# Optimization experiments

Hardware: AMD Instinct MI355X
Metric: run time of the kernel (lower is better)

Reference implementation:

```python
import jax, jax.numpy as jnp
import numpy as np

GROUPS = 8
EPS = 1e-5
PERM_IN = {'x': (0, 2, 4, 1, 3), 'y': (0, 2, 3, 1, 4), 'seq': (0, 3, 4, 1, 2)}
PERM_OUT = {'x': (0, 3, 1, 4, 2), 'y': (0, 3, 1, 2, 4), 'seq': (0, 3, 4, 1, 2)}


def bn_train(x, gamma, beta, axis=1):
    """Training-mode batch norm: normalize over all axes except `axis`."""
    axes = tuple(i for i in range(x.ndim) if i != axis)
    mean = x.mean(axes, keepdims=True)
    var = x.var(axes, keepdims=True)
    shp = [1] * x.ndim
    shp[axis] = x.shape[axis]
    return (x - mean) * jax.lax.rsqrt(var + EPS) * gamma.reshape(shp) + beta.reshape(shp)


def axial_attn(x, qkv_w, gq, bq, gs, bs, go, bo, direction):
    # x: (N, C, seq, H, W)
    x = jnp.transpose(x, PERM_IN[direction])
    N, seq, W, C, H = x.shape
    B = N * seq * W
    xf = x.reshape(B, C, H)
    # 1x1 conv1d qkv projection + BN over channels
    qkv = jnp.einsum('oc,bch->boh', qkv_w, xf)            # (B, 2C, H)
    qkv = bn_train(qkv, gq, bq, axis=1)
    gp = C // GROUPS                                       # group_planes
    qkv = qkv.reshape(B, GROUPS, 2 * gp, H)
    q = qkv[:, :, : gp // 2]
    k = qkv[:, :, gp // 2: gp]
    v = qkv[:, :, gp:]
    qk = jnp.einsum('bgci,bgcj->bgij', q, k)               # (B, g, H, H)
    qk = bn_train(qk, gs, bs, axis=1)
    sim = jax.nn.softmax(qk, axis=3)
    sv = jnp.einsum('bgij,bgcj->bgci', sim, v)             # (B, g, gp, H)
    sv = bn_train(sv.reshape(B, C, H), go, bo, axis=1)
    out = sv.reshape(N, seq, W, C, H)
    return jnp.transpose(out, PERM_OUT[direction])


def setup_inputs() -> dict:
    key = jax.random.key(0)
    ks = jax.random.split(key, 4)
    N, C_in, seq, H, W = 2, 128, 16, 56, 56
    width = 64
    x = jax.random.normal(ks[0], (N, C_in, seq, H, W), jnp.float32)
    cd_w = jax.random.normal(ks[1], (width, C_in), jnp.float32) * (1.0 / np.sqrt(C_in))
    qkv_w = jax.random.normal(ks[2], (3, 2 * width, width), jnp.float32) * (1.0 / np.sqrt(width))
    cu_w = jax.random.normal(ks[3], (2 * width, width), jnp.float32) * (1.0 / np.sqrt(width))
    return {
        'x': x,
        'cd_w': cd_w,
        'bn1_g': jnp.ones((width,), jnp.float32),
        'bn1_b': jnp.zeros((width,), jnp.float32),
        'qkv_w': qkv_w,
        'bnq_g': jnp.ones((3, 2 * width), jnp.float32),
        'bnq_b': jnp.zeros((3, 2 * width), jnp.float32),
        'bns_g': jnp.ones((3, GROUPS), jnp.float32),
        'bns_b': jnp.zeros((3, GROUPS), jnp.float32),
        'bno_g': jnp.ones((3, width), jnp.float32),
        'bno_b': jnp.zeros((3, width), jnp.float32),
        'cu_w': cu_w,
        'bn2_g': jnp.ones((2 * width,), jnp.float32),
        'bn2_b': jnp.zeros((2 * width,), jnp.float32),
    }


def reference(x, cd_w, bn1_g, bn1_b, qkv_w, bnq_g, bnq_b, bns_g, bns_b,
              bno_g, bno_b, cu_w, bn2_g, bn2_b):
    identity = x
    out = jnp.einsum('oc,ncshw->noshw', cd_w, x)           # conv_down (1x1)
    out = jax.nn.relu(bn_train(out, bn1_g, bn1_b, axis=1))
    for i, d in enumerate(('x', 'y', 'seq')):              # height, width, seq axial passes
        out = axial_attn(out, qkv_w[i], bnq_g[i], bnq_b[i], bns_g[i], bns_b[i],
                         bno_g[i], bno_b[i], d)
    out = jax.nn.relu(out)
    out = jnp.einsum('oc,ncshw->noshw', cu_w, out)         # conv_up (1x1)
    out = bn_train(out, bn2_g, bn2_b, axis=1)
    return jax.nn.relu(out + identity)
```

## Files before the change

kernel.cpp:

```cpp
#include <hip/hip_runtime.h>

constexpr int SP = 16*56*56;
constexpr int P  = 2*SP;
constexpr float EPSV = 1e-5f;
constexpr float INVP = 1.f/100352.f;

constexpr size_t SZ_A   = (size_t)2*64*SP;
constexpr size_t OFF_A  = 0;
constexpr size_t OFF_C  = SZ_A;
constexpr size_t OFF_ST = OFF_C + SZ_A;
constexpr size_t OFF_P1 = 0;
constexpr size_t OFF_P2 = 65536;

__global__ void __launch_bounds__(256) kern_down(
    const float* __restrict__ x, const float* __restrict__ w,
    float* __restrict__ A, float* __restrict__ st)
{
  __shared__ float xs[128*64];
  __shared__ float wt[64*129];
  __shared__ float ssum[64], ssq[64];
  const int t = threadIdx.x;
  if (t < 64) { ssum[t] = 0.f; ssq[t] = 0.f; }
  const int p0 = blockIdx.x * 64;
  const int n = p0 / SP, rem = p0 % SP;
  const float* xb = x + (size_t)n*128*SP + rem;
  for (int e4 = t; e4 < 128*16; e4 += 256) {
    int c = e4 >> 4, p4 = (e4 & 15)*4;
    float4 v = *reinterpret_cast<const float4*>(xb + (size_t)c*SP + p4);
    *reinterpret_cast<float4*>(&xs[c*64 + p4]) = v;
  }
  for (int e4 = t; e4 < 64*32; e4 += 256) {
    int o = e4 >> 5, c4 = (e4 & 31)*4;
    float4 v = *reinterpret_cast<const float4*>(w + o*128 + c4);
    *reinterpret_cast<float4*>(&wt[o*129 + c4]) = v;
  }
  __syncthreads();
  const int og = t & 15, pg = t >> 4;
  float acc[4][4] = {};
  for (int c = 0; c < 128; ++c) {
    float xv[4], wv[4];
    #pragma unroll
    for (int j = 0; j < 4; ++j) xv[j] = xs[c*64 + pg*4 + j];
    #pragma unroll
    for (int i = 0; i < 4; ++i) wv[i] = wt[(og + 16*i)*129 + c];
    #pragma unroll
    for (int i = 0; i < 4; ++i) {
      #pragma unroll
      for (int j = 0; j < 4; ++j) acc[i][j] = fmaf(wv[i], xv[j], acc[i][j]);
    }
  }
  float* Ab = A + (size_t)n*64*SP + rem;
  #pragma unroll
  for (int i = 0; i < 4; ++i) {
    const int o = og + 16*i;
    float s1 = 0.f, s2 = 0.f;
    #pragma unroll
    for (int j = 0; j < 4; ++j) { float v = acc[i][j]; s1 += v; s2 += v*v; }
    float4 v4 = make_float4(acc[i][0], acc[i][1], acc[i][2], acc[i][3]);
    *reinterpret_cast<float4*>(Ab + (size_t)o*SP + pg*4) = v4;
    atomicAdd(&ssum[o], s1);
    atomicAdd(&ssq[o], s2);
  }
  __syncthreads();
  if (t < 64) { atomicAdd(&st[t], ssum[t]); atomicAdd(&st[64+t], ssq[t]); }
}

__global__ void __launch_bounds__(256) kern_tr(
    const float* __restrict__ A, float* __restrict__ At)
{
  __shared__ float tile[56*57];
  const size_t base = (size_t)blockIdx.x*3136;
  for (int e4 = threadIdx.x; e4 < 784; e4 += 256) {
    int e = e4*4, h = e/56, w = e%56;
    float4 v = *reinterpret_cast<const float4*>(A + base + e);
    tile[w*57+h] = v.x; tile[(w+1)*57+h] = v.y;
    tile[(w+2)*57+h] = v.z; tile[(w+3)*57+h] = v.w;
  }
  __syncthreads();
  for (int e4 = threadIdx.x; e4 < 784; e4 += 256) {
    int e = e4*4, w = e/56, h = e%56;
    float4 v = make_float4(tile[w*57+h], tile[w*57+h+1], tile[w*57+h+2], tile[w*57+h+3]);
    *reinterpret_cast<float4*>(At + base + e) = v;
  }
}

__global__ void __launch_bounds__(256) kern_tr2(
    const float* __restrict__ A, float* __restrict__ At2)
{
  __shared__ float tile[16*785];
  const int bid = blockIdx.x;
  const int slice = bid >> 2, hw0 = (bid & 3)*784;
  const float* Asrc = A + (size_t)slice*SP + hw0;
  for (int e4 = threadIdx.x; e4 < 3136; e4 += 256) {
    int s = e4/196, h4 = (e4%196)*4;
    float4 v = *reinterpret_cast<const float4*>(Asrc + (size_t)s*3136 + h4);
    tile[s*785 + h4]   = v.x; tile[s*785 + h4+1] = v.y;
    tile[s*785 + h4+2] = v.z; tile[s*785 + h4+3] = v.w;
  }
  __syncthreads();
  float* dst = At2 + ((size_t)slice*3136 + hw0)*16;
  for (int hw = threadIdx.x; hw < 784; hw += 256) {
    #pragma unroll
    for (int sq = 0; sq < 4; ++sq) {
      float4 v = make_float4(tile[(4*sq)*785 + hw], tile[(4*sq+1)*785 + hw],
                             tile[(4*sq+2)*785 + hw], tile[(4*sq+3)*785 + hw]);
      *reinterpret_cast<float4*>(dst + (size_t)hw*16 + sq*4) = v;
    }
  }
}

__global__ void __launch_bounds__(256) kern_up(
    const float* __restrict__ A, const float* __restrict__ w,
    float* __restrict__ U, float* __restrict__ st)
{
  __shared__ float xs[64*64];
  __shared__ float wt[128*65];
  __shared__ float ssum[128], ssq[128];
  const int t = threadIdx.x;
  if (t < 128) { ssum[t]=0.f; ssq[t]=0.f; }
  const int p0 = blockIdx.x*64;
  const int n = p0/SP, rem = p0%SP;
  const float* Ab = A + (size_t)n*64*SP + rem;
  for (int e4 = t; e4 < 64*16; e4 += 256) {
    int c = e4 >> 4, p4 = (e4 & 15)*4;
    float4 v = *reinterpret_cast<const float4*>(Ab + (size_t)c*SP + p4);
    v.x = fmaxf(v.x, 0.f); v.y = fmaxf(v.y, 0.f); v.z = fmaxf(v.z, 0.f); v.w = fmaxf(v.w, 0.f);
    *reinterpret_cast<float4*>(&xs[c*64 + p4]) = v;
  }
  for (int e4 = t; e4 < 128*16; e4 += 256) {
    int o = e4 >> 4, c4 = (e4 & 15)*4;
    float4 v = *reinterpret_cast<const float4*>(w + o*64 + c4);
    *reinterpret_cast<float4*>(&wt[o*65 + c4]) = v;
  }
  __syncthreads();
  const int og = t & 31, pg = t >> 5;
  float acc[4][8] = {};
  for (int c = 0; c < 64; ++c) {
    float xv[8];
    #pragma unroll
    for (int j = 0; j < 8; ++j) xv[j] = xs[c*64 + pg*8 + j];
    #pragma unroll
    for (int i = 0; i < 4; ++i) {
      float wv = wt[(og + 32*i)*65 + c];
      #pragma unroll
      for (int j = 0; j < 8; ++j) acc[i][j] = fmaf(wv, xv[j], acc[i][j]);
    }
  }
  float* Ub = U + (size_t)n*128*SP + rem;
  #pragma unroll
  for (int i = 0; i < 4; ++i) {
    const int o = og + 32*i;
    float s1=0.f, s2=0.f;
    #pragma unroll
    for (int j = 0; j < 8; ++j) { float v = acc[i][j]; s1 += v; s2 += v*v; }
    float4 a = make_float4(acc[i][0],acc[i][1],acc[i][2],acc[i][3]);
    float4 b = make_float4(acc[i][4],acc[i][5],acc[i][6],acc[i][7]);
    *reinterpret_cast<float4*>(Ub + (size_t)o*SP + pg*8)     = a;
    *reinterpret_cast<float4*>(Ub + (size_t)o*SP + pg*8 + 4) = b;
    atomicAdd(&ssum[o], s1); atomicAdd(&ssq[o], s2);
  }
  __syncthreads();
  if (t < 128) { atomicAdd(&st[t], ssum[t]); atomicAdd(&st[128+t], ssq[t]); }
}

template<bool FIRST>
__global__ void __launch_bounds__(256) kern_qkv(
    const float* __restrict__ src, const float* __restrict__ w,
    const float* __restrict__ st1, const float* __restrict__ g1,
    const float* __restrict__ b1,
    float* __restrict__ Bq, float* __restrict__ st)
{
  constexpr int H = 56;
  __shared__ float xs[64*H];
  __shared__ float wt[128*65];
  __shared__ float ssum[128], ssq[128];
  __shared__ float sc1s[64], sh1s[64];
  const int t = threadIdx.x;
  if (t < 128) { ssum[t]=0.f; ssq[t]=0.f; }
  if (FIRST) {
    if (t < 64) {
      float mean = st1[t]*INVP;
      float var  = st1[64+t]*INVP - mean*mean;
      float sc   = g1[t]*rsqrtf(var + EPSV);
      sc1s[t] = sc; sh1s[t] = b1[t] - mean*sc;
    }
    __syncthreads();
  }
  const int b = blockIdx.x;
  const int n = b/896, r = b%896, s = r/56, q = r%56;
  const size_t base = (size_t)n*64*SP + s*3136 + q*56;
  for (int e4 = t; e4 < 64*14; e4 += 256) {
    int c = e4/14, j4 = (e4%14)*4;
    float4 v = *reinterpret_cast<const float4*>(src + base + (size_t)c*SP + j4);
    if (FIRST) {
      float sc = sc1s[c], sh = sh1s[c];
      v.x = fmaxf(fmaf(v.x, sc, sh), 0.f); v.y = fmaxf(fmaf(v.y, sc, sh), 0.f);
      v.z = fmaxf(fmaf(v.z, sc, sh), 0.f); v.w = fmaxf(fmaf(v.w, sc, sh), 0.f);
    }
    xs[c*H + j4]   = v.x; xs[c*H + j4+1] = v.y;
    xs[c*H + j4+2] = v.z; xs[c*H + j4+3] = v.w;
  }
  for (int e4 = t; e4 < 128*16; e4 += 256) {
    int o = e4 >> 4, c4 = (e4 & 15)*4;
    float4 v = *reinterpret_cast<const float4*>(w + o*64 + c4);
    *reinterpret_cast<float4*>(&wt[o*65 + c4]) = v;
  }
  __syncthreads();
  const int og = t & 31, hg = t >> 5;
  float acc[4][7] = {};
  for (int c = 0; c < 64; ++c) {
    float xv[7];
    #pragma unroll
    for (int j = 0; j < 7; ++j) xv[j] = xs[c*H + hg*7 + j];
    #pragma unroll
    for (int i = 0; i < 4; ++i) {
      float wv = wt[(og + 32*i)*65 + c];
      #pragma unroll
      for (int j = 0; j < 7; ++j) acc[i][j] = fmaf(wv, xv[j], acc[i][j]);
    }
  }
  float* ob = Bq + (size_t)b*128*H;
  #pragma unroll
  for (int i = 0; i < 4; ++i) {
    const int o = og + 32*i;
    float s1=0.f, s2=0.f;
    #pragma unroll
    for (int j = 0; j < 7; ++j) {
      float v = acc[i][j];
      ob[o*H + hg*7 + j] = v;
      s1 += v; s2 += v*v;
    }
    atomicAdd(&ssum[o], s1); atomicAdd(&ssq[o], s2);
  }
  __syncthreads();
  if (t < 128) { atomicAdd(&st[t], ssum[t]); atomicAdd(&st[128+t], ssq[t]); }
}

__global__ void __launch_bounds__(256) kern_qkv2(
    const float* __restrict__ At2, const float* __restrict__ w,
    float* __restrict__ Bq, float* __restrict__ st)
{
  __shared__ float xs[64*64];
  __shared__ float wt[128*65];
  __shared__ float ssum[128], ssq[128];
  const int t = threadIdx.x;
  if (t < 128) { ssum[t]=0.f; ssq[t]=0.f; }
  const int b = blockIdx.x;
  const int n = b/784, r = b%784, y = r/14, w4 = (r%14)*4;
  for (int e4 = t; e4 < 1024; e4 += 256) {
    int c = e4 >> 4, rr = e4 & 15, wl = rr >> 2, s4 = (rr & 3)*4;
    float4 v = *reinterpret_cast<const float4*>(
        At2 + (((size_t)(n*64+c)*3136) + y*56 + w4 + wl)*16 + s4);
    *reinterpret_cast<float4*>(&xs[c*64 + wl*16 + s4]) = v;
  }
  for (int e4 = t; e4 < 128*16; e4 += 256) {
    int o = e4 >> 4, c4 = (e4 & 15)*4;
    float4 v = *reinterpret_cast<const float4*>(w + o*64 + c4);
    *reinterpret_cast<float4*>(&wt[o*65 + c4]) = v;
  }
  __syncthreads();
  const int og = t & 31, cg = t >> 5;
  float acc[4][8] = {};
  for (int c = 0; c < 64; ++c) {
    float xv[8];
    #pragma unroll
    for (int j = 0; j < 8; ++j) xv[j] = xs[c*64 + cg*8 + j];
    #pragma unroll
    for (int i = 0; i < 4; ++i) {
      float wv = wt[(og + 32*i)*65 + c];
      #pragma unroll
      for (int j = 0; j < 8; ++j) acc[i][j] = fmaf(wv, xv[j], acc[i][j]);
    }
  }
  const size_t b0 = (size_t)n*3136 + (size_t)y*56 + w4;
  #pragma unroll
  for (int i = 0; i < 4; ++i) {
    const int o = og + 32*i;
    float s1=0.f, s2=0.f;
    #pragma unroll
    for (int j = 0; j < 8; ++j) {
      int col = cg*8 + j, wl = col >> 4, s = col & 15;
      float v = acc[i][j];
      Bq[(b0 + wl)*2048 + o*16 + s] = v;
      s1 += v; s2 += v*v;
    }
    atomicAdd(&ssum[o], s1); atomicAdd(&ssq[o], s2);
  }
  __syncthreads();
  if (t < 128) { atomicAdd(&st[t], ssum[t]); atomicAdd(&st[128+t], ssq[t]); }
}

__global__ void __launch_bounds__(256) kern_redfin(
    const float* __restrict__ part, const float* __restrict__ g,
    const float* __restrict__ b, float* __restrict__ scsh,
    int nb, int nch, float invc)
{
  const int ch = blockIdx.x;
  const int t = threadIdx.x;
  float s1 = 0.f, s2 = 0.f;
  for (int i = t; i < nb; i += 256) {
    s1 += part[(size_t)i*2*nch + ch];
    s2 += part[(size_t)i*2*nch + nch + ch];
  }
  #pragma unroll
  for (int off = 32; off >= 1; off >>= 1) { s1 += __shfl_xor(s1, off); s2 += __shfl_xor(s2, off); }
  __shared__ float r1[4], r2[4];
  if ((t & 63) == 0) { r1[t>>6] = s1; r2[t>>6] = s2; }
  __syncthreads();
  if (t == 0) {
    float S1 = r1[0]+r1[1]+r1[2]+r1[3], S2 = r2[0]+r2[1]+r2[2]+r2[3];
    float mean = S1*invc, var = S2*invc - mean*mean;
    float sc = g[ch]*rsqrtf(var + EPSV);
    scsh[ch] = sc;
    scsh[nch + ch] = b[ch] - mean*sc;
  }
}

template<int H>
__global__ void __launch_bounds__(256) kern_pass1(
    const float* __restrict__ Bq, const float* __restrict__ stq,
    const float* __restrict__ gq, const float* __restrict__ bq,
    float* __restrict__ part)
{
  constexpr int PW = (H==16) ? 4 : 1;
  const int t = threadIdx.x;
  const int wave = t >> 6, lane = t & 63;
  const int sub = (PW==1) ? 0 : (lane >> 4);
  const int i = (PW==1) ? lane : (lane & 15);
  __shared__ float kls[4][4*H*PW];
  __shared__ float bs[16];
  __shared__ float qscs[128], qshs[128];
  if (t < 16) bs[t] = 0.f;
  if (t < 128) {
    float mean = stq[t]*INVP;
    float var  = stq[128+t]*INVP - mean*mean;
    float sc   = gq[t]*rsqrtf(var + EPSV);
    qscs[t] = sc; qshs[t] = bq[t] - mean*sc;
  }
  __syncthreads();
  float* klw = kls[wave];
  const int pair0 = (blockIdx.x*4 + wave)*PW;
  for (int e = lane; e < 4*H*PW; e += 64) {
    int sp = e / (4*H), r = e % (4*H);
    int c = r / H, j = r % H;
    int pr = pair0 + sp, bb = pr >> 3, g = pr & 7;
    int o = g*16 + 4 + c;
    klw[e] = fmaf(Bq[((size_t)bb*128 + o)*H + j], qscs[o], qshs[o]);
  }
  __syncthreads();
  const int pr = pair0 + sub, bb = pr >> 3, g = pr & 7;
  const float* kp = klw + sub*4*H;
  const bool act = (i < H);
  float q[4];
  #pragma unroll
  for (int c = 0; c < 4; ++c) {
    int o = g*16 + c;
    q[c] = act ? fmaf(Bq[((size_t)bb*128 + o)*H + i], qscs[o], qshs[o]) : 0.f;
  }
  float s1 = 0.f, s2 = 0.f;
  #pragma unroll
  for (int j = 0; j < H; ++j) {
    float s = q[0]*kp[j] + q[1]*kp[H+j] + q[2]*kp[2*H+j] + q[3]*kp[3*H+j];
    s1 += s; s2 += s*s;
  }
  #pragma unroll
  for (int off = (PW==1?32:8); off >= 1; off >>= 1) {
    s1 += __shfl_xor(s1, off);
    s2 += __shfl_xor(s2, off);
  }
  if ((lane & (PW==1?63:15)) == 0) { atomicAdd(&bs[g], s1); atomicAdd(&bs[8+g], s2); }
  __syncthreads();
  if (t < 16) part[(size_t)blockIdx.x*16 + t] = bs[t];
}

template<int H>
__global__ void __launch_bounds__(256) kern_attn(
    const float* __restrict__ Bq, const float* __restrict__ stq,
    const float* __restrict__ gq, const float* __restrict__ bq,
    const float* __restrict__ ssc,
    float* __restrict__ C, float* __restrict__ part)
{
  constexpr int PW = (H==16) ? 4 : 1;
  const int t = threadIdx.x;
  const int wave = t >> 6, lane = t & 63;
  const int sub = (PW==1) ? 0 : (lane >> 4);
  const int i = (PW==1) ? lane : (lane & 15);
  __shared__ float kv[4][12*H*PW];
  __shared__ float bsum[64], bsq[64];
  __shared__ float qscs[128], qshs[128];
  if (t < 64) { bsum[t] = 0.f; bsq[t] = 0.f; }
  if (t < 128) {
    float mean = stq[t]*INVP;
    float var  = stq[128+t]*INVP - mean*mean;
    float sc   = gq[t]*rsqrtf(var + EPSV);
    qscs[t] = sc; qshs[t] = bq[t] - mean*sc;
  }
  __syncthreads();
  float* kvw = kv[wave];
  const int pair0 = (blockIdx.x*4 + wave)*PW;
  for (int e = lane; e < 12*H*PW; e += 64) {
    int sp = e / (12*H), r = e % (12*H);
    int c = r / H, j = r % H;
    int pr = pair0 + sp, bb = pr >> 3, g = pr & 7;
    int o = g*16 + 4 + c;
    kvw[e] = fmaf(Bq[((size_t)bb*128 + o)*H + j], qscs[o], qshs[o]);
  }
  __syncthreads();
  const int pr = pair0 + sub, bb = pr >> 3, g = pr & 7;
  const float* kp = kvw + sub*12*H;
  const bool act = (i < H);
  float q[4];
  #pragma unroll
  for (int c = 0; c < 4; ++c) {
    int o = g*16 + c;
    q[c] = act ? fmaf(Bq[((size_t)bb*128 + o)*H + i], qscs[o], qshs[o]) : 0.f;
  }
  const float As = ssc[g];
  float m = -3.4e38f;
  for (int j = 0; j < H; ++j) {
    float s = As * (q[0]*kp[j] + q[1]*kp[H+j] + q[2]*kp[2*H+j] + q[3]*kp[3*H+j]);
    m = fmaxf(m, s);
  }
  float den = 0.f;
  float acc[8] = {};
  for (int j = 0; j < H; ++j) {
    float s = As * (q[0]*kp[j] + q[1]*kp[H+j] + q[2]*kp[2*H+j] + q[3]*kp[3*H+j]);
    float e = __expf(s - m);
    den += e;
    #pragma unroll
    for (int c = 0; c < 8; ++c) acc[c] = fmaf(e, kp[(4+c)*H + j], acc[c]);
  }
  const float inv = 1.f/den;
  #pragma unroll
  for (int c = 0; c < 8; ++c) {
    float vv = act ? acc[c]*inv : 0.f;
    if (act) C[((size_t)bb*64 + g*8 + c)*H + i] = vv;
    float s1 = vv, s2 = vv*vv;
    #pragma unroll
    for (int off = (PW==1?32:8); off >= 1; off >>= 1) {
      s1 += __shfl_xor(s1, off);
      s2 += __shfl_xor(s2, off);
    }
    if ((lane & (PW==1?63:15)) == 0) { atomicAdd(&bsum[g*8+c], s1); atomicAdd(&bsq[g*8+c], s2); }
  }
  __syncthreads();
  if (t < 64) {
    part[(size_t)blockIdx.x*128 + t]      = bsum[t];
    part[(size_t)blockIdx.x*128 + 64 + t] = bsq[t];
  }
}

__global__ void __launch_bounds__(256) kern_scat0(
    const float* __restrict__ C, const float* __restrict__ osc,
    const float* __restrict__ osh, float* __restrict__ A)
{
  __shared__ float tile[56*57];
  const int bid = blockIdx.x;
  const int c = bid & 63, s = (bid >> 6) & 15, n = bid >> 10;
  const float sc = osc[c], sh = osh[c];
  const size_t cb = ((size_t)(n*16+s)*56)*3584 + c*56;
  for (int e = threadIdx.x; e < 3136; e += 256) {
    int w = e/56, h = e%56;
    tile[w*57+h] = C[cb + (size_t)w*3584 + h];
  }
  __syncthreads();
  const size_t ab = ((size_t)(n*64+c)*16+s)*3136;
  for (int e = threadIdx.x; e < 3136; e += 256) {
    int h = e/56, w = e%56;
    A[ab + e] = fmaf(tile[w*57+h], sc, sh);
  }
}

__global__ void __launch_bounds__(256) kern_scat1(
    const float* __restrict__ C, const float* __restrict__ osc,
    const float* __restrict__ osh, float* __restrict__ A)
{
  const int e4 = blockIdx.x*256 + threadIdx.x;
  if (e4 >= 1792*64*14) return;
  const int w4 = (e4 % 14)*4, c = (e4/14) & 63, b = e4 / (14*64);
  const int n = b/896, r = b%896, s = r/56, y = r%56;
  const float sc = osc[c], sh = osh[c];
  float4 v = *reinterpret_cast<const float4*>(C + ((size_t)b*64 + c)*56 + w4);
  v.x = fmaf(v.x, sc, sh); v.y = fmaf(v.y, sc, sh);
  v.z = fmaf(v.z, sc, sh); v.w = fmaf(v.w, sc, sh);
  *reinterpret_cast<float4*>(A + ((size_t)(n*64+c)*16+s)*3136 + y*56 + w4) = v;
}

__global__ void __launch_bounds__(256) kern_scat2(
    const float* __restrict__ C, const float* __restrict__ osc,
    const float* __restrict__ osh, float* __restrict__ A)
{
  __shared__ float tile[56*17];
  const int bid = blockIdx.x;
  const int y = bid % 56, c = (bid/56) & 63, n = bid / 3584;
  const float sc = osc[c], sh = osh[c];
  const size_t cb = ((size_t)(n*56+y)*56)*1024 + c*16;
  for (int e = threadIdx.x; e < 896; e += 256) {
    int w = e >> 4, s = e & 15;
    tile[w*17+s] = C[cb + (size_t)w*1024 + s];
  }
  __syncthreads();
  const size_t ab = (size_t)(n*64+c)*16*3136 + y*56;
  for (int e = threadIdx.x; e < 896; e += 256) {
    int s = e/56, w = e%56;
    A[ab + (size_t)s*3136 + w] = fmaf(tile[w*17+s], sc, sh);
  }
}

__global__ void __launch_bounds__(256) kern_final(
    float* __restrict__ U, const float* __restrict__ x,
    const float* __restrict__ st2, const float* __restrict__ g2,
    const float* __restrict__ b2, float* __restrict__ out)
{
  __shared__ float scs[128], shs[128];
  const int t = threadIdx.x;
  if (t < 128) {
    float mean = st2[t]*INVP;
    float var  = st2[128+t]*INVP - mean*mean;
    float sc   = g2[t]*rsqrtf(var + EPSV);
    scs[t] = sc; shs[t] = b2[t] - mean*sc;
  }
  __syncthreads();
  const int idx = blockIdx.x*256 + t;
  if (idx >= P*128/4) return;
  const int e = idx*4;
  const int o = (e / SP) & 127;
  float4 u  = *reinterpret_cast<const float4*>(U + e);
  float4 xv = *reinterpret_cast<const float4*>(x + e);
  const float s = scs[o], h = shs[o];
  float4 r;
  r.x = fmaxf(fmaf(u.x, s, h) + xv.x, 0.f);
  r.y = fmaxf(fmaf(u.y, s, h) + xv.y, 0.f);
  r.z = fmaxf(fmaf(u.z, s, h) + xv.z, 0.f);
  r.w = fmaxf(fmaf(u.w, s, h) + xv.w, 0.f);
  *reinterpret_cast<float4*>(out + e) = r;
}

extern "C" void kernel_launch(void* const* d_in, const int* in_sizes, int n_in,
                              void* d_out, int out_size, void* d_ws, size_t ws_size,
                              hipStream_t stream)
{
  const float* x    = (const float*)d_in[0];
  const float* cdw  = (const float*)d_in[1];
  const float* bn1g = (const float*)d_in[2];
  const float* bn1b = (const float*)d_in[3];
  const float* qkvw = (const float*)d_in[4];
  const float* bnqg = (const float*)d_in[5];
  const float* bnqb = (const float*)d_in[6];
  const float* bnsg = (const float*)d_in[7];
  const float* bnsb = (const float*)d_in[8];
  const float* bnog = (const float*)d_in[9];
  const float* bnob = (const float*)d_in[10];
  const float* cuw  = (const float*)d_in[11];
  const float* bn2g = (const float*)d_in[12];
  const float* bn2b = (const float*)d_in[13];
  float* out = (float*)d_out;
  float* ws  = (float*)d_ws;

  float* A   = ws + OFF_A;
  float* C   = ws + OFF_C;
  float* st  = ws + OFF_ST;
  float* Pp1 = ws + OFF_P1;
  float* Pp2 = ws + OFF_P2;
  float* Bq  = out;

  hipMemsetAsync(st, 0, 4096*sizeof(float), stream);

  kern_down<<<P/64, 256, 0, stream>>>(x, cdw, A, st);

  {
    float* stq = st + 256; float* sts = stq + 512; float* sto = stq + 544;
    kern_tr<<<2048, 256, 0, stream>>>(A, C);
    kern_qkv<true><<<1792, 256, 0, stream>>>(C, qkvw, st, bn1g, bn1b, Bq, stq);
    kern_pass1<56><<<3584, 256, 0, stream>>>(Bq, stq, bnqg, bnqb, Pp1);
    kern_redfin<<<8, 256, 0, stream>>>(Pp1, bnsg, bnsb, sts, 3584, 8, 1.f/5619712.f);
    kern_attn<56><<<3584, 256, 0, stream>>>(Bq, stq, bnqg, bnqb, sts, C, Pp2);
    kern_redfin<<<64, 256, 0, stream>>>(Pp2, bnog, bnob, sto, 3584, 64, INVP);
    kern_scat0<<<2048, 256, 0, stream>>>(C, sto, sto+64, A);
  }
  {
    float* stq = st + 256 + 1024; float* sts = stq + 512; float* sto = stq + 544;
    kern_qkv<false><<<1792, 256, 0, stream>>>(A, qkvw+8192, st, bn1g, bn1b, Bq, stq);
    kern_pass1<56><<<3584, 256, 0, stream>>>(Bq, stq, bnqg+128, bnqb+128, Pp1);
    kern_redfin<<<8, 256, 0, stream>>>(Pp1, bnsg+8, bnsb+8, sts, 3584, 8, 1.f/5619712.f);
    kern_attn<56><<<3584, 256, 0, stream>>>(Bq, stq, bnqg+128, bnqb+128, sts, C, Pp2);
    kern_redfin<<<64, 256, 0, stream>>>(Pp2, bnog+64, bnob+64, sto, 3584, 64, INVP);
    kern_scat1<<<6272, 256, 0, stream>>>(C, sto, sto+64, A);
  }
  {
    float* stq = st + 256 + 2048; float* sts = stq + 512; float* sto = stq + 544;
    kern_tr2<<<512, 256, 0, stream>>>(A, C);
    kern_qkv2<<<1568, 256, 0, stream>>>(C, qkvw+16384, Bq, stq);
    kern_pass1<16><<<3136, 256, 0, stream>>>(Bq, stq, bnqg+256, bnqb+256, Pp1);
    kern_redfin<<<8, 256, 0, stream>>>(Pp1, bnsg+16, bnsb+16, sts, 3136, 8, 1.f/1605632.f);
    kern_attn<16><<<3136, 256, 0, stream>>>(Bq, stq, bnqg+256, bnqb+256, sts, C, Pp2);
    kern_redfin<<<64, 256, 0, stream>>>(Pp2, bnog+128, bnob+128, sto, 3136, 64, INVP);
    kern_scat2<<<7168, 256, 0, stream>>>(C, sto, sto+64, A);
  }

  float* st2 = st + 3328;
  kern_up<<<P/64, 256, 0, stream>>>(A, cuw, Bq, st2);
  kern_final<<<P*128/4/256, 256, 0, stream>>>(Bq, x, st2, bn2g, bn2b, out);
}
```

Baseline: 651.1 us.

## Split channel reduction into two chunks to shrink shared memory in GEMM kernels

Four 1x1-conv style GEMM kernels (down, up, qkv, qkv2) now stage inputs and weights in two halves along the reduction dimension instead of all at once, roughly halving LDS per block. The aim is to fit more blocks per CU and hide global-load latency through higher occupancy. In exchange each block performs an extra pair of barriers and reloads, with no overlap between loading and compute inside a block. The weight stores into padded LDS also become scalar because of the odd stride.

Result: faster. 636.2 us (-2.3%).

```diff
diff --git a/kernel.cpp b/kernel.cpp
--- a/kernel.cpp
+++ b/kernel.cpp
@@ -16,37 +16,41 @@
     const float* __restrict__ x, const float* __restrict__ w,
     float* __restrict__ A, float* __restrict__ st)
 {
-  __shared__ float xs[128*64];
-  __shared__ float wt[64*129];
+  __shared__ float xs[64*64];
+  __shared__ float wt[64*65];
   __shared__ float ssum[64], ssq[64];
   const int t = threadIdx.x;
   if (t < 64) { ssum[t] = 0.f; ssq[t] = 0.f; }
   const int p0 = blockIdx.x * 64;
   const int n = p0 / SP, rem = p0 % SP;
   const float* xb = x + (size_t)n*128*SP + rem;
-  for (int e4 = t; e4 < 128*16; e4 += 256) {
-    int c = e4 >> 4, p4 = (e4 & 15)*4;
-    float4 v = *reinterpret_cast<const float4*>(xb + (size_t)c*SP + p4);
-    *reinterpret_cast<float4*>(&xs[c*64 + p4]) = v;
-  }
-  for (int e4 = t; e4 < 64*32; e4 += 256) {
-    int o = e4 >> 5, c4 = (e4 & 31)*4;
-    float4 v = *reinterpret_cast<const float4*>(w + o*128 + c4);
-    *reinterpret_cast<float4*>(&wt[o*129 + c4]) = v;
-  }
-  __syncthreads();
   const int og = t & 15, pg = t >> 4;
   float acc[4][4] = {};
-  for (int c = 0; c < 128; ++c) {
-    float xv[4], wv[4];
-    #pragma unroll
-    for (int j = 0; j < 4; ++j) xv[j] = xs[c*64 + pg*4 + j];
-    #pragma unroll
-    for (int i = 0; i < 4; ++i) wv[i] = wt[(og + 16*i)*129 + c];
-    #pragma unroll
-    for (int i = 0; i < 4; ++i) {
-      #pragma unroll
-      for (int j = 0; j < 4; ++j) acc[i][j] = fmaf(wv[i], xv[j], acc[i][j]);
+  for (int ck = 0; ck < 2; ++ck) {
+    __syncthreads();
+    for (int e4 = t; e4 < 64*16; e4 += 256) {
+      int c = e4 >> 4, p4 = (e4 & 15)*4;
+      float4 v = *reinterpret_cast<const float4*>(xb + (size_t)(ck*64+c)*SP + p4);
+      *reinterpret_cast<float4*>(&xs[c*64 + p4]) = v;
+    }
+    for (int e4 = t; e4 < 64*16; e4 += 256) {
+      int o = e4 >> 4, c4 = (e4 & 15)*4;
+      float4 v = *reinterpret_cast<const float4*>(w + o*128 + ck*64 + c4);
+      wt[o*65 + c4]   = v.x; wt[o*65 + c4+1] = v.y;
+      wt[o*65 + c4+2] = v.z; wt[o*65 + c4+3] = v.w;
+    }
+    __syncthreads();
+    for (int c = 0; c < 64; ++c) {
+      float xv[4], wv[4];
+      #pragma unroll
+      for (int j = 0; j < 4; ++j) xv[j] = xs[c*64 + pg*4 + j];
+      #pragma unroll
+      for (int i = 0; i < 4; ++i) wv[i] = wt[(og + 16*i)*65 + c];
+      #pragma unroll
+      for (int i = 0; i < 4; ++i) {
+        #pragma unroll
+        for (int j = 0; j < 4; ++j) acc[i][j] = fmaf(wv[i], xv[j], acc[i][j]);
+      }
     }
   }
   float* Ab = A + (size_t)n*64*SP + rem;
@@ -113,37 +117,41 @@
     const float* __restrict__ A, const float* __restrict__ w,
     float* __restrict__ U, float* __restrict__ st)
 {
-  __shared__ float xs[64*64];
-  __shared__ float wt[128*65];
+  __shared__ float xs[32*64];
+  __shared__ float wt[128*33];
   __shared__ float ssum[128], ssq[128];
   const int t = threadIdx.x;
   if (t < 128) { ssum[t]=0.f; ssq[t]=0.f; }
   const int p0 = blockIdx.x*64;
   const int n = p0/SP, rem = p0%SP;
   const float* Ab = A + (size_t)n*64*SP + rem;
-  for (int e4 = t; e4 < 64*16; e4 += 256) {
-    int c = e4 >> 4, p4 = (e4 & 15)*4;
-    float4 v = *reinterpret_cast<const float4*>(Ab + (size_t)c*SP + p4);
-    v.x = fmaxf(v.x, 0.f); v.y = fmaxf(v.y, 0.f); v.z = fmaxf(v.z, 0.f); v.w = fmaxf(v.w, 0.f);
-    *reinterpret_cast<float4*>(&xs[c*64 + p4]) = v;
-  }
-  for (int e4 = t; e4 < 128*16; e4 += 256) {
-    int o = e4 >> 4, c4 = (e4 & 15)*4;
-    float4 v = *reinterpret_cast<const float4*>(w + o*64 + c4);
-    *reinterpret_cast<float4*>(&wt[o*65 + c4]) = v;
-  }
-  __syncthreads();
   const int og = t & 31, pg = t >> 5;
   float acc[4][8] = {};
-  for (int c = 0; c < 64; ++c) {
-    float xv[8];
-    #pragma unroll
-    for (int j = 0; j < 8; ++j) xv[j] = xs[c*64 + pg*8 + j];
-    #pragma unroll
-    for (int i = 0; i < 4; ++i) {
-      float wv = wt[(og + 32*i)*65 + c];
-      #pragma unroll
-      for (int j = 0; j < 8; ++j) acc[i][j] = fmaf(wv, xv[j], acc[i][j]);
+  for (int ck = 0; ck < 2; ++ck) {
+    __syncthreads();
+    for (int e4 = t; e4 < 32*16; e4 += 256) {
+      int c = e4 >> 4, p4 = (e4 & 15)*4;
+      float4 v = *reinterpret_cast<const float4*>(Ab + (size_t)(ck*32+c)*SP + p4);
+      v.x = fmaxf(v.x, 0.f); v.y = fmaxf(v.y, 0.f); v.z = fmaxf(v.z, 0.f); v.w = fmaxf(v.w, 0.f);
+      *reinterpret_cast<float4*>(&xs[c*64 + p4]) = v;
+    }
+    for (int e4 = t; e4 < 128*8; e4 += 256) {
+      int o = e4 >> 3, c4 = (e4 & 7)*4;
+      float4 v = *reinterpret_cast<const float4*>(w + o*64 + ck*32 + c4);
+      wt[o*33 + c4]   = v.x; wt[o*33 + c4+1] = v.y;
+      wt[o*33 + c4+2] = v.z; wt[o*33 + c4+3] = v.w;
+    }
+    __syncthreads();
+    for (int c = 0; c < 32; ++c) {
+      float xv[8];
+      #pragma unroll
+      for (int j = 0; j < 8; ++j) xv[j] = xs[c*64 + pg*8 + j];
+      #pragma unroll
+      for (int i = 0; i < 4; ++i) {
+        float wv = wt[(og + 32*i)*33 + c];
+        #pragma unroll
+        for (int j = 0; j < 8; ++j) acc[i][j] = fmaf(wv, xv[j], acc[i][j]);
+      }
     }
   }
   float* Ub = U + (size_t)n*128*SP + rem;
@@ -171,52 +179,53 @@
     float* __restrict__ Bq, float* __restrict__ st)
 {
   constexpr int H = 56;
-  __shared__ float xs[64*H];
-  __shared__ float wt[128*65];
+  __shared__ float xs[32*H];
+  __shared__ float wt[128*33];
   __shared__ float ssum[128], ssq[128];
   __shared__ float sc1s[64], sh1s[64];
   const int t = threadIdx.x;
   if (t < 128) { ssum[t]=0.f; ssq[t]=0.f; }
-  if (FIRST) {
-    if (t < 64) {
-      float mean = st1[t]*INVP;
-      float var  = st1[64+t]*INVP - mean*mean;
-      float sc   = g1[t]*rsqrtf(var + EPSV);
-      sc1s[t] = sc; sh1s[t] = b1[t] - mean*sc;
-    }
-    __syncthreads();
+  if (FIRST && t < 64) {
+    float mean = st1[t]*INVP;
+    float var  = st1[64+t]*INVP - mean*mean;
+    float sc   = g1[t]*rsqrtf(var + EPSV);
+    sc1s[t] = sc; sh1s[t] = b1[t] - mean*sc;
   }
   const int b = blockIdx.x;
   const int n = b/896, r = b%896, s = r/56, q = r%56;
   const size_t base = (size_t)n*64*SP + s*3136 + q*56;
-  for (int e4 = t; e4 < 64*14; e4 += 256) {
-    int c = e4/14, j4 = (e4%14)*4;
-    float4 v = *reinterpret_cast<const float4*>(src + base + (size_t)c*SP + j4);
-    if (FIRST) {
-      float sc = sc1s[c], sh = sh1s[c];
-      v.x = fmaxf(fmaf(v.x, sc, sh), 0.f); v.y = fmaxf(fmaf(v.y, sc, sh), 0.f);
-      v.z = fmaxf(fmaf(v.z, sc, sh), 0.f); v.w = fmaxf(fmaf(v.w, sc, sh), 0.f);
-    }
-    xs[c*H + j4]   = v.x; xs[c*H + j4+1] = v.y;
-    xs[c*H + j4+2] = v.z; xs[c*H + j4+3] = v.w;
-  }
-  for (int e4 = t; e4 < 128*16; e4 += 256) {
-    int o = e4 >> 4, c4 = (e4 & 15)*4;
-    float4 v = *reinterpret_cast<const float4*>(w + o*64 + c4);
-    *reinterpret_cast<float4*>(&wt[o*65 + c4]) = v;
-  }
-  __syncthreads();
   const int og = t & 31, hg = t >> 5;
   float acc[4][7] = {};
-  for (int c = 0; c < 64; ++c) {
-    float xv[7];
-    #pragma unroll
-    for (int j = 0; j < 7; ++j) xv[j] = xs[c*H + hg*7 + j];
-    #pragma unroll
-    for (int i = 0; i < 4; ++i) {
-      float wv = wt[(og + 32*i)*65 + c];
-      #pragma unroll
-      for (int j = 0; j < 7; ++j) acc[i][j] = fmaf(wv, xv[j], acc[i][j]);
+  for (int ck = 0; ck < 2; ++ck) {
+    __syncthreads();
+    for (int e4 = t; e4 < 32*14; e4 += 256) {
+      int c = e4/14, j4 = (e4%14)*4;
+      float4 v = *reinterpret_cast<const float4*>(src + base + (size_t)(ck*32+c)*SP + j4);
+      if (FIRST) {
+        float sc = sc1s[ck*32+c], sh = sh1s[ck*32+c];
+        v.x = fmaxf(fmaf(v.x, sc, sh), 0.f); v.y = fmaxf(fmaf(v.y, sc, sh), 0.f);
+        v.z = fmaxf(fmaf(v.z, sc, sh), 0.f); v.w = fmaxf(fmaf(v.w, sc, sh), 0.f);
+      }
+      xs[c*H + j4]   = v.x; xs[c*H + j4+1] = v.y;
+      xs[c*H + j4+2] = v.z; xs[c*H + j4+3] = v.w;
+    }
+    for (int e4 = t; e4 < 128*8; e4 += 256) {
+      int o = e4 >> 3, c4 = (e4 & 7)*4;
+      float4 v = *reinterpret_cast<const float4*>(w + o*64 + ck*32 + c4);
+      wt[o*33 + c4]   = v.x; wt[o*33 + c4+1] = v.y;
+      wt[o*33 + c4+2] = v.z; wt[o*33 + c4+3] = v.w;
+    }
+    __syncthreads();
+    for (int c = 0; c < 32; ++c) {
+      float xv[7];
+      #pragma unroll
+      for (int j = 0; j < 7; ++j) xv[j] = xs[c*H + hg*7 + j];
+      #pragma unroll
+      for (int i = 0; i < 4; ++i) {
+        float wv = wt[(og + 32*i)*33 + c];
+        #pragma unroll
+        for (int j = 0; j < 7; ++j) acc[i][j] = fmaf(wv, xv[j], acc[i][j]);
+      }
     }
   }
   float* ob = Bq + (size_t)b*128*H;
@@ -240,36 +249,40 @@
     const float* __restrict__ At2, const float* __restrict__ w,
     float* __restrict__ Bq, float* __restrict__ st)
 {
-  __shared__ float xs[64*64];
-  __shared__ float wt[128*65];
+  __shared__ float xs[32*64];
+  __shared__ float wt[128*33];
   __shared__ float ssum[128], ssq[128];
   const int t = threadIdx.x;
   if (t < 128) { ssum[t]=0.f; ssq[t]=0.f; }
   const int b = blockIdx.x;
   const int n = b/784, r = b%784, y = r/14, w4 = (r%14)*4;
-  for (int e4 = t; e4 < 1024; e4 += 256) {
-    int c = e4 >> 4, rr = e4 & 15, wl = rr >> 2, s4 = (rr & 3)*4;
-    float4 v = *reinterpret_cast<const float4*>(
-        At2 + (((size_t)(n*64+c)*3136) + y*56 + w4 + wl)*16 + s4);
-    *reinterpret_cast<float4*>(&xs[c*64 + wl*16 + s4]) = v;
-  }
-  for (int e4 = t; e4 < 128*16; e4 += 256) {
-    int o = e4 >> 4, c4 = (e4 & 15)*4;
-    float4 v = *reinterpret_cast<const float4*>(w + o*64 + c4);
-    *reinterpret_cast<float4*>(&wt[o*65 + c4]) = v;
-  }
-  __syncthreads();
   const int og = t & 31, cg = t >> 5;
   float acc[4][8] = {};
-  for (int c = 0; c < 64; ++c) {
-    float xv[8];
-    #pragma unroll
-    for (int j = 0; j < 8; ++j) xv[j] = xs[c*64 + cg*8 + j];
-    #pragma unroll
-    for (int i = 0; i < 4; ++i) {
-      float wv = wt[(og + 32*i)*65 + c];
-      #pragma unroll
-      for (int j = 0; j < 8; ++j) acc[i][j] = fmaf(wv, xv[j], acc[i][j]);
+  for (int ck = 0; ck < 2; ++ck) {
+    __syncthreads();
+    for (int e4 = t; e4 < 512; e4 += 256) {
+      int c = e4 >> 4, rr = e4 & 15, wl = rr >> 2, s4 = (rr & 3)*4;
+      float4 v = *reinterpret_cast<const float4*>(
+          At2 + (((size_t)(n*64 + ck*32 + c)*3136) + y*56 + w4 + wl)*16 + s4);
+      *reinterpret_cast<float4*>(&xs[c*64 + wl*16 + s4]) = v;
+    }
+    for (int e4 = t; e4 < 128*8; e4 += 256) {
+      int o = e4 >> 3, c4 = (e4 & 7)*4;
+      float4 v = *reinterpret_cast<const float4*>(w + o*64 + ck*32 + c4);
+      wt[o*33 + c4]   = v.x; wt[o*33 + c4+1] = v.y;
+      wt[o*33 + c4+2] = v.z; wt[o*33 + c4+3] = v.w;
+    }
+    __syncthreads();
+    for (int c = 0; c < 32; ++c) {
+      float xv[8];
+      #pragma unroll
+      for (int j = 0; j < 8; ++j) xv[j] = xs[c*64 + cg*8 + j];
+      #pragma unroll
+      for (int i = 0; i < 4; ++i) {
+        float wv = wt[(og + 32*i)*33 + c];
+        #pragma unroll
+        for (int j = 0; j < 8; ++j) acc[i][j] = fmaf(wv, xv[j], acc[i][j]);
+      }
     }
   }
   const size_t b0 = (size_t)n*3136 + (size_t)y*56 + w4;
```
